# Kernel optimization log

Measured on AMD Instinct MI355X. Metric: run time of the kernel, lower is better.

Reference implementation:

```python
import jax, jax.numpy as jnp
import numpy as np


def setup_inputs() -> dict:
    key = jax.random.key(0)
    k1, k2 = jax.random.split(key)
    B, N, M = 4, 16384, 4096
    src_points = jax.random.normal(k1, (B, N, 3), dtype=jnp.float32)
    target_verts = jax.random.normal(k2, (B, M, 3), dtype=jnp.float32)
    return {"src_points": src_points, "target_verts": target_verts}


def reference(src_points, target_verts):
    # target_faces=None path of ChamferLoss: degenerate one-vertex triangles,
    # so closest-point-on-mesh == nearest target vertex.
    # d2[b,n,m] = ||p_bn - v_bm||^2 via the expansion p2 + v2 - 2 p.v
    p2 = jnp.sum(src_points * src_points, axis=-1)          # (B, N)
    v2 = jnp.sum(target_verts * target_verts, axis=-1)      # (B, M)
    pv = jnp.einsum('bnd,bmd->bnm', src_points, target_verts)  # (B, N, M)
    d2 = p2[:, :, None] + v2[:, None, :] - 2.0 * pv
    d2 = jnp.maximum(d2, 0.0)
    min_d2 = jnp.min(d2, axis=-1)                            # (B, N)
    num_src_per_batch = src_points.shape[1]
    loss = jnp.sum(min_d2, axis=-1) / num_src_per_batch      # (B,)
    return loss
```

## Files before the change

### kernel.cpp

```cpp
#include <hip/hip_runtime.h>
#include <float.h>


typedef __bf16 bf16x8 __attribute__((ext_vector_type(8)));
typedef float  f32x16 __attribute__((ext_vector_type(16)));

constexpr int B = 4, N = 16384, M = 4096;
constexpr int TPB = 256;
constexpr int PPB = 128;
constexpr int NBLK = (B * N) / PPB;
constexpr int PHASES = 8;
constexpr int PHASE_V = M / PHASES;
constexpr int PHASE_TILES = PHASE_V / 32;
constexpr unsigned POISON = 0xAAAAAAAAu;

__device__ __forceinline__ void write_vert(char* bp, int u,
                                           float x, float y, float z) {
    __bf16 xh = (__bf16)x, yh = (__bf16)y, zh = (__bf16)z;
    float xhf = (float)xh, yhf = (float)yh, zhf = (float)zh;
    __bf16 xl = (__bf16)(x - xhf), yl = (__bf16)(y - yhf), zl = (__bf16)(z - zhf);
    float v2 = fmaf(x, x, fmaf(y, y, z * z));
    __bf16 v2h = (__bf16)v2;
    __bf16 v2l = (__bf16)(v2 - (float)v2h);
    __bf16 zero = (__bf16)0.0f;
    bf16x8 h0, h1;
    h0[0] = (__bf16)(-2.0f * xhf); h0[1] = (__bf16)(-2.0f * yhf);
    h0[2] = (__bf16)(-2.0f * zhf);
    h0[3] = h0[0]; h0[4] = h0[1]; h0[5] = h0[2];
    h0[6] = (__bf16)(-2.0f * (float)xl); h0[7] = (__bf16)(-2.0f * (float)yl);
    h1[0] = (__bf16)(-2.0f * (float)zl); h1[1] = v2h; h1[2] = v2l;
    h1[3] = zero; h1[4] = zero; h1[5] = zero; h1[6] = zero; h1[7] = zero;
    char* base = bp + ((u >> 5) << 10) + ((u & 31) << 4);
    *(bf16x8*)base         = h0;
    *(bf16x8*)(base + 512) = h1;
}

__global__ __launch_bounds__(TPB, 2) void chamfer_fused(
    const float* __restrict__ src, const float* __restrict__ tv,
    float* __restrict__ out, float* __restrict__ ws)
{
    __shared__ char buf[2][PHASE_TILES * 1024];
    __shared__ float acc[4];
    __shared__ int flag;

    const int blk  = blockIdx.x;
    const int b    = blk >> 7;
    const int t    = threadIdx.x;
    const int w    = t >> 6, L = t & 63;
    const int half = L >> 5, c = L & 31;

    const int gp = blk * PPB + w * 32 + c;
    float ax = src[3 * gp], ay = src[3 * gp + 1], az = src[3 * gp + 2];
    float pp = fmaf(ax, ax, fmaf(ay, ay, az * az));
    __bf16 one = (__bf16)1.0f, zero = (__bf16)0.0f;
    bf16x8 aA;
    {
        __bf16 xh = (__bf16)ax, yh = (__bf16)ay, zh = (__bf16)az;
        __bf16 xl = (__bf16)(ax - (float)xh), yl = (__bf16)(ay - (float)yh),
               zl = (__bf16)(az - (float)zh);
        if (half == 0) { aA[0]=xh; aA[1]=yh; aA[2]=zh; aA[3]=xl; aA[4]=yl; aA[5]=zl; aA[6]=xh; aA[7]=yh; }
        else { aA[0]=zh; aA[1]=one; aA[2]=one; aA[3]=zero; aA[4]=zero; aA[5]=zero; aA[6]=zero; aA[7]=zero; }
    }

    f32x16 mn, zeroC;
#pragma unroll
    for (int r = 0; r < 16; ++r) { mn[r] = FLT_MAX; zeroC[r] = 0.0f; }

    const float* tvb = tv + (size_t)b * M * 3;
    float r0, r1, r2, r3, r4, r5;
    {
        const float* p = tvb + 6 * t;
        float2 A = *(const float2*)p, Bq = *(const float2*)(p + 2),
               Cq = *(const float2*)(p + 4);
        r0 = A.x; r1 = A.y; r2 = Bq.x; r3 = Bq.y; r4 = Cq.x; r5 = Cq.y;
    }

    for (int phase = 0; phase < PHASES; ++phase) {
        char* bp = buf[phase & 1];
        write_vert(bp, 2 * t,     r0, r1, r2);
        write_vert(bp, 2 * t + 1, r3, r4, r5);
        if (phase + 1 < PHASES) {
            const float* p = tvb + (size_t)(phase + 1) * PHASE_V * 3 + 6 * t;
            float2 A = *(const float2*)p, Bq = *(const float2*)(p + 2),
                   Cq = *(const float2*)(p + 4);
            r0 = A.x; r1 = A.y; r2 = Bq.x; r3 = Bq.y; r4 = Cq.x; r5 = Cq.y;
        }
        __syncthreads();
        const char* rp = bp + half * 512 + c * 16;
#pragma unroll 4
        for (int tl = 0; tl < PHASE_TILES; ++tl) {
            bf16x8 bf = *(const bf16x8*)(rp + tl * 1024);
            f32x16 C = __builtin_amdgcn_mfma_f32_32x32x16_bf16(aA, bf, zeroC, 0, 0, 0);
#pragma unroll
            for (int r = 0; r < 16; ++r) mn[r] = fminf(mn[r], C[r]);
        }
    }

#pragma unroll
    for (int off = 16; off > 0; off >>= 1) {
#pragma unroll
        for (int r = 0; r < 16; ++r)
            mn[r] = fminf(mn[r], __shfl_xor(mn[r], off, 64));
    }
    float s = 0.0f;
#pragma unroll
    for (int r = 0; r < 16; ++r) {
        int row = (r & 3) + 8 * (r >> 2) + 4 * half;
        if (c == row) s = fmaxf(mn[r] + pp, 0.0f);
    }
    for (int off = 32; off > 0; off >>= 1)
        s += __shfl_down(s, off, 64);
    if (L == 0) acc[w] = s;
    __syncthreads();

    if (t == 0) {
        float bs = acc[0] + acc[1] + acc[2] + acc[3];
        unsigned* cnt = (unsigned*)(ws + NBLK);
        atomicExch(&ws[blk], bs);
        __threadfence();
        (void)atomicCAS(cnt, POISON, 0u);
        __threadfence();
        unsigned n = atomicAdd(cnt, 1u);
        flag = (n == NBLK - 1) ? 1 : 0;
    }
    __syncthreads();

    if (flag) {
        float s2 = atomicAdd(&ws[w * 128 + L], 0.0f)
                 + atomicAdd(&ws[w * 128 + 64 + L], 0.0f);
        for (int off = 32; off > 0; off >>= 1)
            s2 += __shfl_down(s2, off, 64);
        if (L == 0) out[w] = s2 * (1.0f / N);
    }
}

extern "C" void kernel_launch(void* const* d_in, const int* in_sizes, int n_in,
                              void* d_out, int out_size, void* d_ws, size_t ws_size,
                              hipStream_t stream) {
    const float* src = (const float*)d_in[0];
    const float* tv  = (const float*)d_in[1];
    float* out = (float*)d_out;
    float* ws  = (float*)d_ws;

    chamfer_fused<<<NBLK, TPB, 0, stream>>>(src, tv, out, ws);
}
```

Baseline: 80.69 us.

## Swap MFMA operands so points map to columns, cut final shuffle reduction

Vertices become the MFMA A operand and points the B operand, so each lane's accumulator column belongs to one source point. The per-tile min can then fold pairs of outputs into 8 registers, and the end-of-kernel reduction needs one cross-half shuffle instead of 80 butterfly shuffles. The vertex staging also drops from 8 double-buffered phases to 2 large single-buffer phases, with loads done directly before a barrier. This removes the prefetch overlap, and the larger LDS footprint may reduce occupancy.

```diff
diff --git a/kernel.cpp b/kernel.cpp
--- a/kernel.cpp
+++ b/kernel.cpp
@@ -6,10 +6,11 @@
 typedef float  f32x16 __attribute__((ext_vector_type(16)));
 
 constexpr int B = 4, N = 16384, M = 4096;
+constexpr int BN = B * N;
 constexpr int TPB = 256;
 constexpr int PPB = 128;
-constexpr int NBLK = (B * N) / PPB;
-constexpr int PHASES = 8;
+constexpr int NBLK = BN / PPB;
+constexpr int PHASES = 2;
 constexpr int PHASE_V = M / PHASES;
 constexpr int PHASE_TILES = PHASE_V / 32;
 constexpr unsigned POISON = 0xAAAAAAAAu;
@@ -39,7 +40,7 @@
     const float* __restrict__ src, const float* __restrict__ tv,
     float* __restrict__ out, float* __restrict__ ws)
 {
-    __shared__ char buf[2][PHASE_TILES * 1024];
+    __shared__ char lds[PHASE_TILES * 1024];
     __shared__ float acc[4];
     __shared__ int flag;
 
@@ -53,61 +54,51 @@
     float ax = src[3 * gp], ay = src[3 * gp + 1], az = src[3 * gp + 2];
     float pp = fmaf(ax, ax, fmaf(ay, ay, az * az));
     __bf16 one = (__bf16)1.0f, zero = (__bf16)0.0f;
-    bf16x8 aA;
+    bf16x8 bP;
     {
         __bf16 xh = (__bf16)ax, yh = (__bf16)ay, zh = (__bf16)az;
         __bf16 xl = (__bf16)(ax - (float)xh), yl = (__bf16)(ay - (float)yh),
                zl = (__bf16)(az - (float)zh);
-        if (half == 0) { aA[0]=xh; aA[1]=yh; aA[2]=zh; aA[3]=xl; aA[4]=yl; aA[5]=zl; aA[6]=xh; aA[7]=yh; }
-        else { aA[0]=zh; aA[1]=one; aA[2]=one; aA[3]=zero; aA[4]=zero; aA[5]=zero; aA[6]=zero; aA[7]=zero; }
+        if (half == 0) { bP[0]=xh; bP[1]=yh; bP[2]=zh; bP[3]=xl; bP[4]=yl; bP[5]=zl; bP[6]=xh; bP[7]=yh; }
+        else { bP[0]=zh; bP[1]=one; bP[2]=one; bP[3]=zero; bP[4]=zero; bP[5]=zero; bP[6]=zero; bP[7]=zero; }
     }
 
-    f32x16 mn, zeroC;
+    float mn[8];
+    f32x16 zeroC;
 #pragma unroll
-    for (int r = 0; r < 16; ++r) { mn[r] = FLT_MAX; zeroC[r] = 0.0f; }
+    for (int u = 0; u < 8; ++u) mn[u] = FLT_MAX;
+#pragma unroll
+    for (int r = 0; r < 16; ++r) zeroC[r] = 0.0f;
 
+    const int laneoff = half * 512 + c * 16;
     const float* tvb = tv + (size_t)b * M * 3;
-    float r0, r1, r2, r3, r4, r5;
-    {
-        const float* p = tvb + 6 * t;
-        float2 A = *(const float2*)p, Bq = *(const float2*)(p + 2),
-               Cq = *(const float2*)(p + 4);
-        r0 = A.x; r1 = A.y; r2 = Bq.x; r3 = Bq.y; r4 = Cq.x; r5 = Cq.y;
-    }
 
-    for (int phase = 0; phase < PHASES; ++phase) {
-        char* bp = buf[phase & 1];
-        write_vert(bp, 2 * t,     r0, r1, r2);
-        write_vert(bp, 2 * t + 1, r3, r4, r5);
-        if (phase + 1 < PHASES) {
-            const float* p = tvb + (size_t)(phase + 1) * PHASE_V * 3 + 6 * t;
-            float2 A = *(const float2*)p, Bq = *(const float2*)(p + 2),
-                   Cq = *(const float2*)(p + 4);
-            r0 = A.x; r1 = A.y; r2 = Bq.x; r3 = Bq.y; r4 = Cq.x; r5 = Cq.y;
+    for (int ph = 0; ph < PHASES; ++ph) {
+        if (ph) __syncthreads();
+        const float* vs = tvb + (size_t)ph * PHASE_V * 3;
+#pragma unroll
+        for (int k = 0; k < 8; ++k) {
+            int u = k * 256 + t;
+            const float* p = vs + 3 * u;
+            write_vert(lds, u, p[0], p[1], p[2]);
         }
         __syncthreads();
-        const char* rp = bp + half * 512 + c * 16;
+
 #pragma unroll 4
         for (int tl = 0; tl < PHASE_TILES; ++tl) {
-            bf16x8 bf = *(const bf16x8*)(rp + tl * 1024);
-            f32x16 C = __builtin_amdgcn_mfma_f32_32x32x16_bf16(aA, bf, zeroC, 0, 0, 0);
+            bf16x8 av = *(const bf16x8*)(lds + tl * 1024 + laneoff);
+            f32x16 C = __builtin_amdgcn_mfma_f32_32x32x16_bf16(av, bP, zeroC, 0, 0, 0);
 #pragma unroll
-            for (int r = 0; r < 16; ++r) mn[r] = fminf(mn[r], C[r]);
+            for (int u = 0; u < 8; ++u)
+                mn[u] = fminf(fminf(mn[u], C[2 * u]), C[2 * u + 1]);
         }
     }
 
-#pragma unroll
-    for (int off = 16; off > 0; off >>= 1) {
-#pragma unroll
-        for (int r = 0; r < 16; ++r)
-            mn[r] = fminf(mn[r], __shfl_xor(mn[r], off, 64));
-    }
-    float s = 0.0f;
-#pragma unroll
-    for (int r = 0; r < 16; ++r) {
-        int row = (r & 3) + 8 * (r >> 2) + 4 * half;
-        if (c == row) s = fmaxf(mn[r] + pp, 0.0f);
-    }
+    float m01 = fminf(fminf(mn[0], mn[1]), fminf(mn[2], mn[3]));
+    float m23 = fminf(fminf(mn[4], mn[5]), fminf(mn[6], mn[7]));
+    float m = fminf(m01, m23);
+    m = fminf(m, __shfl_xor(m, 32, 64));
+    float s = (L < 32) ? fmaxf(m + pp, 0.0f) : 0.0f;
     for (int off = 32; off > 0; off >>= 1)
         s += __shfl_down(s, off, 64);
     if (L == 0) acc[w] = s;
```

New measurement: 78.81 us. -2.3%, faster.
